# Optimization experiments

Measured on AMD Instinct MI355X. Metric: run time of the kernel, lower is better.

The kernel has to match this reference:

```python
import jax, jax.numpy as jnp
import numpy as np

K, D = 512, 64
B, H, W = 32, 64, 64


def setup_inputs() -> dict:
    key = jax.random.key(0)
    k1, k2 = jax.random.split(key)
    z_e_x = jax.random.normal(k1, (B, D, H, W), dtype=jnp.float32)
    # nn.Embedding weight initialized uniform(-1/K, 1/K)
    codebook = jax.random.uniform(k2, (K, D), dtype=jnp.float32,
                                  minval=-1.0 / K, maxval=1.0 / K)
    return {"z_e_x": z_e_x, "codebook": codebook}


def _quantize_indices(flat, codebook):
    # distances[n,k] = ||c_k||^2 + ||x_n||^2 - 2 x_n . c_k  (addmm form)
    cb_sqr = jnp.sum(codebook * codebook, axis=1)            # [K]
    x_sqr = jnp.sum(flat * flat, axis=1, keepdims=True)      # [N,1]
    distances = cb_sqr + x_sqr - 2.0 * (flat @ codebook.T)   # [N,K]
    return jnp.argmin(distances, axis=1)                     # [N]


def reference(z_e_x, codebook):
    # VQEmbedding.straight_through forward: returns (z_q_x, z_q_x_bar), both NCHW.
    b, d, h, w = z_e_x.shape
    x = jnp.transpose(z_e_x, (0, 2, 3, 1))       # NHWC
    flat = x.reshape(-1, d)                      # [N,D]
    idx = _quantize_indices(flat, codebook)      # [N]
    codes = jnp.take(codebook, idx, axis=0).reshape(b, h, w, d)
    z_q = jnp.transpose(codes, (0, 3, 1, 2))     # NCHW
    # z_q_x (detached codebook path) and z_q_x_bar (live codebook path) are
    # numerically identical in the forward pass.
    return (z_q, z_q)
```

## Files before the change

### kernel.cpp

```cpp
#include <hip/hip_runtime.h>


typedef short bf16x8 __attribute__((ext_vector_type(8)));
typedef float f32x4  __attribute__((ext_vector_type(4)));

#define KCODES 512
#define DDIM 64
#define HWSZ 4096
#define NPOS 131072
#define POSB 128
#define NBLK (NPOS / POSB)
#define OUT2_OFF 8388608
#define S_X 129

__device__ __forceinline__ unsigned short f2bf_rne(float f) {
    unsigned u = __builtin_bit_cast(unsigned, f);
    unsigned r = u + 0x7FFFu + ((u >> 16) & 1u);
    return (unsigned short)(r >> 16);
}
__device__ __forceinline__ float bf2f(unsigned short h) {
    unsigned u = ((unsigned)h) << 16;
    return __builtin_bit_cast(float, u);
}

__device__ __forceinline__ float np_sumsq64(const float* __restrict__ a) {
#pragma clang fp contract(off)
    float r0 = a[0]*a[0], r1 = a[1]*a[1], r2 = a[2]*a[2], r3 = a[3]*a[3];
    float r4 = a[4]*a[4], r5 = a[5]*a[5], r6 = a[6]*a[6], r7 = a[7]*a[7];
#pragma unroll
    for (int i = 8; i < 64; i += 8) {
        r0 += a[i+0]*a[i+0]; r1 += a[i+1]*a[i+1];
        r2 += a[i+2]*a[i+2]; r3 += a[i+3]*a[i+3];
        r4 += a[i+4]*a[i+4]; r5 += a[i+5]*a[i+5];
        r6 += a[i+6]*a[i+6]; r7 += a[i+7]*a[i+7];
    }
    return ((r0+r1)+(r2+r3)) + ((r4+r5)+(r6+r7));
}

__global__ __launch_bounds__(256) void vq_prep(
    const float* __restrict__ cb, unsigned short* __restrict__ wsb,
    float* __restrict__ wscb)
{
    if (blockIdx.x < 128) {
        int u = blockIdx.x * 256 + threadIdx.x;
        int k = u >> 6, d = u & 63;
        float c = cb[u];
        unsigned short ch = f2bf_rne(c);
        float clf = c - bf2f(ch);
        unsigned short cl = f2bf_rne(clf);
        int tile = k >> 4, n = k & 15;
        int chunk = d >> 5, quad = (d >> 3) & 3, j = d & 7;
        int lane = quad * 16 + n;
        size_t base = ((((size_t)tile*2 + chunk)*2 + 0)*64 + lane)*8 + j;
        wsb[base]       = (unsigned short)ch;
        wsb[base + 512] = (unsigned short)cl;
    } else {
        int k = (blockIdx.x - 128) * 256 + threadIdx.x;
        if (k < KCODES) wscb[k] = np_sumsq64(cb + k * DDIM);
    }
}

__global__ __launch_bounds__(256, 4) void vq_main(
    const float* __restrict__ z, const float* __restrict__ cb,
    const unsigned short* __restrict__ wsb, const float* __restrict__ wscb,
    float* __restrict__ out)
{
#pragma clang fp contract(off)
    __shared__ float s_regA[64 * S_X];
    __shared__ float s_cbsqr[KCODES];
    __shared__ float s_xsqr[POSB];
    __shared__ float s_part[2 * POSB];
    __shared__ int   s_idx[POSB];
    __shared__ int   s_flist[POSB];
    __shared__ int   s_cnt;

    const int tid = threadIdx.x;
    const int wv = tid >> 6, ln = tid & 63;
    const int m = ln & 15, q = ln >> 4;
    const int n0 = blockIdx.x * POSB;
    const long gbase = (long)(n0 >> 12) * (DDIM * HWSZ) + (n0 & 4095);

    if (tid == 0) s_cnt = 0;
    s_cbsqr[tid] = wscb[tid];
    s_cbsqr[tid + 256] = wscb[tid + 256];

#pragma unroll
    for (int i = 0; i < 32; ++i) {
        int d = wv * 16 + (i & 15), ph = i >> 4;
        s_regA[d * S_X + ph * 64 + ln] = z[gbase + (long)d * HWSZ + ph * 64 + ln];
    }
    __syncthreads();

    {
        int p = tid & 127, h = tid >> 7;
        float r0 = 0.f, r1 = 0.f, r2 = 0.f, r3 = 0.f;
#pragma unroll
        for (int i = 0; i < 8; ++i) {
            float a0 = s_regA[(8*i + 4*h + 0) * S_X + p];
            float a1 = s_regA[(8*i + 4*h + 1) * S_X + p];
            float a2 = s_regA[(8*i + 4*h + 2) * S_X + p];
            float a3 = s_regA[(8*i + 4*h + 3) * S_X + p];
            r0 += a0*a0; r1 += a1*a1; r2 += a2*a2; r3 += a3*a3;
        }
        s_part[h * POSB + p] = (r0 + r1) + (r2 + r3);
    }

    bf16x8 Ah[4], Al[4];
#pragma unroll
    for (int rt = 0; rt < 2; ++rt)
#pragma unroll
        for (int c = 0; c < 2; ++c) {
            int pos = wv * 32 + rt * 16 + m;
            bf16x8 ah, al;
#pragma unroll
            for (int j = 0; j < 8; ++j) {
                float xv = s_regA[(c*32 + q*8 + j) * S_X + pos];
                unsigned short hh = f2bf_rne(xv);
                float lo = xv - bf2f(hh);
                ah[j] = (short)hh;
                al[j] = (short)f2bf_rne(lo);
            }
            Ah[rt*2 + c] = ah; Al[rt*2 + c] = al;
        }
    __syncthreads();
    if (tid < POSB) s_xsqr[tid] = s_part[tid] + s_part[POSB + tid];

    float m1[8], m2[8]; int t1[8];
#pragma unroll
    for (int i = 0; i < 8; ++i) { m1[i] = 3.4e38f; m2[i] = 3.4e38f; t1[i] = 0; }

    for (int g = 0; g < 4; ++g) {
        __syncthreads();
        const float4* src = (const float4*)wsb + g * 2048;
        float4* dst = (float4*)s_regA;
#pragma unroll
        for (int i = 0; i < 8; ++i) dst[i * 256 + tid] = src[i * 256 + tid];
        __syncthreads();

        const unsigned short* sb = (const unsigned short*)s_regA;
        for (int ti = 0; ti < 8; ++ti) {
            int t = g * 8 + ti;
            bf16x8 Bh0 = *(const bf16x8*)(sb + ((ti*2+0)*2+0)*512 + ln*8);
            bf16x8 Bl0 = *(const bf16x8*)(sb + ((ti*2+0)*2+1)*512 + ln*8);
            bf16x8 Bh1 = *(const bf16x8*)(sb + ((ti*2+1)*2+0)*512 + ln*8);
            bf16x8 Bl1 = *(const bf16x8*)(sb + ((ti*2+1)*2+1)*512 + ln*8);
            float cbv = s_cbsqr[t * 16 + m];
#pragma unroll
            for (int rt = 0; rt < 2; ++rt) {
                f32x4 acc = {0.f, 0.f, 0.f, 0.f};
                acc = __builtin_amdgcn_mfma_f32_16x16x32_bf16(Al[rt*2+0], Bh0, acc, 0,0,0);
                acc = __builtin_amdgcn_mfma_f32_16x16x32_bf16(Ah[rt*2+0], Bl0, acc, 0,0,0);
                acc = __builtin_amdgcn_mfma_f32_16x16x32_bf16(Ah[rt*2+0], Bh0, acc, 0,0,0);
                acc = __builtin_amdgcn_mfma_f32_16x16x32_bf16(Al[rt*2+1], Bh1, acc, 0,0,0);
                acc = __builtin_amdgcn_mfma_f32_16x16x32_bf16(Ah[rt*2+1], Bl1, acc, 0,0,0);
                acc = __builtin_amdgcn_mfma_f32_16x16x32_bf16(Ah[rt*2+1], Bh1, acc, 0,0,0);
#pragma unroll
                for (int r = 0; r < 4; ++r) {
                    float sc = fmaf(-2.f, acc[r], cbv);
                    int cell = rt * 4 + r;
                    bool lt = sc < m1[cell];
                    m2[cell] = fminf(m2[cell], lt ? m1[cell] : sc);
                    if (lt) { m1[cell] = sc; t1[cell] = t; }
                }
            }
        }
    }

#pragma unroll
    for (int cell = 0; cell < 8; ++cell) {
        int rt = cell >> 2, r = cell & 3;
        float v1 = m1[cell], v2 = m2[cell];
        int i1 = t1[cell] * 16 + m;
#pragma unroll
        for (int s = 1; s < 16; s <<= 1) {
            float o1 = __shfl_xor(v1, s);
            float o2 = __shfl_xor(v2, s);
            int   oi = __shfl_xor(i1, s);
            bool take = (o1 < v1) || (o1 == v1 && oi < i1);
            float lose = take ? v1 : o1;
            if (take) { v1 = o1; i1 = oi; }
            v2 = fminf(fminf(v2, o2), lose);
        }
        if (m == 0) {
            int pos = wv * 32 + rt * 16 + q * 4 + r;
            float xs = s_xsqr[pos];
            float sx = 8.0f * sqrtf(xs) * 1.01f;
            float amax = 0.00196f * sx + 0.01f;
            float eps = 1.5f * (3.0f * 1.52587890625e-5f * 0.00196f * sx
                                + 500.f * 5.96e-8f * amax);
            float delta = 2.4e-7f * (xs + 1.0f) + 64.f * 1.2e-7f * amax;
            float W = 2.f * eps + 2.f * delta + 1e-9f;
            int flag = (v2 - v1 <= W) ? (1 << 30) : 0;
            s_idx[pos] = i1 | flag;
        }
    }
    __syncthreads();
    if (tid < POSB) {
        if (s_idx[tid] & (1 << 30)) {
            int slot = atomicAdd(&s_cnt, 1);
            s_flist[slot] = tid;
        }
    }
    __syncthreads();

    const int cnt = s_cnt;
    for (int i = wv; i < cnt; i += 4) {
        int p = __builtin_amdgcn_readfirstlane(s_flist[i]);
        float xv = z[gbase + (long)ln * HWSZ + p];
        float xs = s_xsqr[p];
        float dot[8];
#pragma unroll
        for (int j = 0; j < 8; ++j) dot[j] = 0.f;
        const float* crow = cb + (ln * 8) * DDIM;
        for (int dc = 0; dc < 16; ++dc) {
            float x0 = __shfl(xv, dc*4 + 0);
            float x1 = __shfl(xv, dc*4 + 1);
            float x2 = __shfl(xv, dc*4 + 2);
            float x3 = __shfl(xv, dc*4 + 3);
#pragma unroll
            for (int j = 0; j < 8; ++j) {
                float4 cv = *(const float4*)(crow + j * DDIM + dc * 4);
                dot[j] = fmaf(x0, cv.x, dot[j]);
                dot[j] = fmaf(x1, cv.y, dot[j]);
                dot[j] = fmaf(x2, cv.z, dot[j]);
                dot[j] = fmaf(x3, cv.w, dot[j]);
            }
        }
        float bv = 3.4e38f; int bi = 0;
#pragma unroll
        for (int j = 0; j < 8; ++j) {
            int k = ln * 8 + j;
            float tt = s_cbsqr[k] + xs;
            float e = fmaf(-2.f, dot[j], tt);
            if (e < bv) { bv = e; bi = k; }
        }
#pragma unroll
        for (int s = 1; s < 64; s <<= 1) {
            float ov = __shfl_xor(bv, s); int oi = __shfl_xor(bi, s);
            if (ov < bv || (ov == bv && oi < bi)) { bv = ov; bi = oi; }
        }
        if (ln == 0) s_idx[p] = bi;
    }
    __syncthreads();

    {
        int p = tid & 127, hf = tid >> 7;
        int idx = s_idx[p] & 0x3FFFFFFF;
        const float4* crow4 = (const float4*)(cb + idx * DDIM + hf * 32);
        float* o0 = out + gbase + p;
        float* o1 = o0 + OUT2_OFF;
#pragma unroll
        for (int qq = 0; qq < 8; ++qq) {
            float4 v = crow4[qq];
            long db = (long)(hf * 32 + qq * 4) * HWSZ;
            o0[db]          = v.x; o0[db + HWSZ]   = v.y;
            o0[db + 2*HWSZ] = v.z; o0[db + 3*HWSZ] = v.w;
            o1[db]          = v.x; o1[db + HWSZ]   = v.y;
            o1[db + 2*HWSZ] = v.z; o1[db + 3*HWSZ] = v.w;
        }
    }
}

extern "C" void kernel_launch(void* const* d_in, const int* in_sizes, int n_in,
                              void* d_out, int out_size, void* d_ws, size_t ws_size,
                              hipStream_t stream) {
    const float* z  = (const float*)d_in[0];
    const float* cb = (const float*)d_in[1];
    float* out = (float*)d_out;
    unsigned short* wsb = (unsigned short*)d_ws;
    float* wscb = (float*)((char*)d_ws + 131072);
    vq_prep<<<130, 256, 0, stream>>>(cb, wsb, wscb);
    vq_main<<<NBLK, 256, 0, stream>>>(z, cb, wsb, wscb, out);
}
```

Measured before the change: 175.1 us.

## Double-buffer codebook tiles via async global-to-LDS loads and split MFMA chains

Replaces the blocking load-then-sync copy of codebook tiles into shared memory with a double-buffered pipeline. Smaller half-size tiles are fetched directly into LDS with global_load_lds while the current tile is consumed. The three-term bf16 split product is also restructured into three independent MFMA accumulation chains that are summed afterwards, shortening the dependency chain. The change alters the summation order and so may shift results slightly. It relies on the async copy landing before the barrier, with no explicit wait on the load counter.

```diff
diff --git a/kernel.cpp b/kernel.cpp
--- a/kernel.cpp
+++ b/kernel.cpp
@@ -21,6 +21,12 @@
 __device__ __forceinline__ float bf2f(unsigned short h) {
     unsigned u = ((unsigned)h) << 16;
     return __builtin_bit_cast(float, u);
+}
+
+__device__ __forceinline__ void async_cp16(const void* g, void* l) {
+    __builtin_amdgcn_global_load_lds(
+        (const __attribute__((address_space(1))) unsigned int*)g,
+        (__attribute__((address_space(3))) unsigned int*)l, 16, 0, 0);
 }
 
 __device__ __forceinline__ float np_sumsq64(const float* __restrict__ a) {
@@ -129,17 +135,28 @@
 #pragma unroll
     for (int i = 0; i < 8; ++i) { m1[i] = 3.4e38f; m2[i] = 3.4e38f; t1[i] = 0; }
 
-    for (int g = 0; g < 4; ++g) {
-        __syncthreads();
-        const float4* src = (const float4*)wsb + g * 2048;
-        float4* dst = (float4*)s_regA;
-#pragma unroll
-        for (int i = 0; i < 8; ++i) dst[i * 256 + tid] = src[i * 256 + tid];
-        __syncthreads();
-
-        const unsigned short* sb = (const unsigned short*)s_regA;
-        for (int ti = 0; ti < 8; ++ti) {
-            int t = g * 8 + ti;
+    {
+        const float4* src = (const float4*)wsb + 0 * 1024;
+        char* dstb = (char*)s_regA + (wv * 64) * 16;
+#pragma unroll
+        for (int i = 0; i < 4; ++i)
+            async_cp16(src + i * 256 + tid, dstb + i * 4096);
+    }
+    __syncthreads();
+
+    for (int g = 0; g < 8; ++g) {
+        if (g < 7) {
+            const float4* src = (const float4*)wsb + (g + 1) * 1024;
+            char* dstb = (char*)s_regA + ((g + 1) & 1) * 16384 + (wv * 64) * 16;
+#pragma unroll
+            for (int i = 0; i < 4; ++i)
+                async_cp16(src + i * 256 + tid, dstb + i * 4096);
+        }
+        const unsigned short* sb =
+            (const unsigned short*)s_regA + (g & 1) * 8192;
+#pragma unroll 2
+        for (int ti = 0; ti < 4; ++ti) {
+            int t = g * 4 + ti;
             bf16x8 Bh0 = *(const bf16x8*)(sb + ((ti*2+0)*2+0)*512 + ln*8);
             bf16x8 Bl0 = *(const bf16x8*)(sb + ((ti*2+0)*2+1)*512 + ln*8);
             bf16x8 Bh1 = *(const bf16x8*)(sb + ((ti*2+1)*2+0)*512 + ln*8);
@@ -147,13 +164,14 @@
             float cbv = s_cbsqr[t * 16 + m];
 #pragma unroll
             for (int rt = 0; rt < 2; ++rt) {
-                f32x4 acc = {0.f, 0.f, 0.f, 0.f};
-                acc = __builtin_amdgcn_mfma_f32_16x16x32_bf16(Al[rt*2+0], Bh0, acc, 0,0,0);
-                acc = __builtin_amdgcn_mfma_f32_16x16x32_bf16(Ah[rt*2+0], Bl0, acc, 0,0,0);
-                acc = __builtin_amdgcn_mfma_f32_16x16x32_bf16(Ah[rt*2+0], Bh0, acc, 0,0,0);
-                acc = __builtin_amdgcn_mfma_f32_16x16x32_bf16(Al[rt*2+1], Bh1, acc, 0,0,0);
-                acc = __builtin_amdgcn_mfma_f32_16x16x32_bf16(Ah[rt*2+1], Bl1, acc, 0,0,0);
-                acc = __builtin_amdgcn_mfma_f32_16x16x32_bf16(Ah[rt*2+1], Bh1, acc, 0,0,0);
+                const f32x4 zac = {0.f, 0.f, 0.f, 0.f};
+                f32x4 aP = __builtin_amdgcn_mfma_f32_16x16x32_bf16(Al[rt*2+0], Bh0, zac, 0,0,0);
+                f32x4 aQ = __builtin_amdgcn_mfma_f32_16x16x32_bf16(Ah[rt*2+0], Bl0, zac, 0,0,0);
+                f32x4 aR = __builtin_amdgcn_mfma_f32_16x16x32_bf16(Ah[rt*2+0], Bh0, zac, 0,0,0);
+                aP = __builtin_amdgcn_mfma_f32_16x16x32_bf16(Al[rt*2+1], Bh1, aP, 0,0,0);
+                aQ = __builtin_amdgcn_mfma_f32_16x16x32_bf16(Ah[rt*2+1], Bl1, aQ, 0,0,0);
+                aR = __builtin_amdgcn_mfma_f32_16x16x32_bf16(Ah[rt*2+1], Bh1, aR, 0,0,0);
+                f32x4 acc = (aP + aQ) + aR;
 #pragma unroll
                 for (int r = 0; r < 4; ++r) {
                     float sc = fmaf(-2.f, acc[r], cbv);
@@ -164,6 +182,7 @@
                 }
             }
         }
+        __syncthreads();
     }
 
 #pragma unroll
```

Result: no change. 178.3 us (+1.8%).

## Restructure VQ kernel to single-wave blocks streaming codebook fragments from global

Applied to the files above, without the earlier changes.

Switches from 256-thread blocks of 128 positions to 64-thread single-wave blocks of 64 positions, each wave covering 4 row tiles. Codebook bf16 fragments are no longer staged in LDS with block barriers; they are loaded straight from global/L2 with one-tile-ahead register prefetch. The input tile is stored position-major with an XOR swizzle to avoid LDS bank conflicts. The three MFMA accumulators run as independent chains to break the dependency. Fallback rescoring now uses a ballot mask instead of an LDS atomic list. In exchange it uses many more registers, launches 4x more blocks, and each wave rereads the whole codebook fragment set from cache.

```diff
diff --git a/kernel.cpp b/kernel.cpp
--- a/kernel.cpp
+++ b/kernel.cpp
@@ -8,10 +8,9 @@
 #define DDIM 64
 #define HWSZ 4096
 #define NPOS 131072
-#define POSB 128
-#define NBLK (NPOS / POSB)
+#define POSW 64
+#define NBLK (NPOS / POSW)
 #define OUT2_OFF 8388608
-#define S_X 129
 
 __device__ __forceinline__ unsigned short f2bf_rne(float f) {
     unsigned u = __builtin_bit_cast(unsigned, f);
@@ -60,114 +59,116 @@
     }
 }
 
-__global__ __launch_bounds__(256, 4) void vq_main(
+__device__ __forceinline__ int xchunk(int p, int c) {
+    return p * 16 + (c ^ (p & 15));
+}
+
+__global__ __launch_bounds__(64, 2) void vq_main(
     const float* __restrict__ z, const float* __restrict__ cb,
     const unsigned short* __restrict__ wsb, const float* __restrict__ wscb,
     float* __restrict__ out)
 {
 #pragma clang fp contract(off)
-    __shared__ float s_regA[64 * S_X];
+    __shared__ float s_x[POSW * DDIM];
     __shared__ float s_cbsqr[KCODES];
-    __shared__ float s_xsqr[POSB];
-    __shared__ float s_part[2 * POSB];
-    __shared__ int   s_idx[POSB];
-    __shared__ int   s_flist[POSB];
-    __shared__ int   s_cnt;
-
-    const int tid = threadIdx.x;
-    const int wv = tid >> 6, ln = tid & 63;
+    __shared__ int   s_idx[POSW];
+
+    const int ln = threadIdx.x;
     const int m = ln & 15, q = ln >> 4;
-    const int n0 = blockIdx.x * POSB;
+    const int n0 = blockIdx.x * POSW;
     const long gbase = (long)(n0 >> 12) * (DDIM * HWSZ) + (n0 & 4095);
-
-    if (tid == 0) s_cnt = 0;
-    s_cbsqr[tid] = wscb[tid];
-    s_cbsqr[tid + 256] = wscb[tid + 256];
-
-#pragma unroll
-    for (int i = 0; i < 32; ++i) {
-        int d = wv * 16 + (i & 15), ph = i >> 4;
-        s_regA[d * S_X + ph * 64 + ln] = z[gbase + (long)d * HWSZ + ph * 64 + ln];
+    float4* s_x4 = (float4*)s_x;
+
+#pragma unroll
+    for (int i = 0; i < 8; ++i) s_cbsqr[i * 64 + ln] = wscb[i * 64 + ln];
+
+#pragma unroll
+    for (int c = 0; c < 16; ++c) {
+        float4 w;
+        w.x = z[gbase + (long)(4*c + 0) * HWSZ + ln];
+        w.y = z[gbase + (long)(4*c + 1) * HWSZ + ln];
+        w.z = z[gbase + (long)(4*c + 2) * HWSZ + ln];
+        w.w = z[gbase + (long)(4*c + 3) * HWSZ + ln];
+        s_x4[xchunk(ln, c)] = w;
     }
     __syncthreads();
 
+    float my_xsqr;
     {
-        int p = tid & 127, h = tid >> 7;
-        float r0 = 0.f, r1 = 0.f, r2 = 0.f, r3 = 0.f;
-#pragma unroll
-        for (int i = 0; i < 8; ++i) {
-            float a0 = s_regA[(8*i + 4*h + 0) * S_X + p];
-            float a1 = s_regA[(8*i + 4*h + 1) * S_X + p];
-            float a2 = s_regA[(8*i + 4*h + 2) * S_X + p];
-            float a3 = s_regA[(8*i + 4*h + 3) * S_X + p];
-            r0 += a0*a0; r1 += a1*a1; r2 += a2*a2; r3 += a3*a3;
-        }
-        s_part[h * POSB + p] = (r0 + r1) + (r2 + r3);
-    }
-
-    bf16x8 Ah[4], Al[4];
-#pragma unroll
-    for (int rt = 0; rt < 2; ++rt)
+        float r0=0.f,r1=0.f,r2=0.f,r3=0.f,r4=0.f,r5=0.f,r6=0.f,r7=0.f;
+#pragma unroll
+        for (int k = 0; k < 8; ++k) {
+            float4 A = s_x4[xchunk(ln, 2*k)];
+            float4 B = s_x4[xchunk(ln, 2*k + 1)];
+            r0 += A.x*A.x; r1 += A.y*A.y; r2 += A.z*A.z; r3 += A.w*A.w;
+            r4 += B.x*B.x; r5 += B.y*B.y; r6 += B.z*B.z; r7 += B.w*B.w;
+        }
+        my_xsqr = ((r0+r1)+(r2+r3)) + ((r4+r5)+(r6+r7));
+    }
+
+    bf16x8 Ah[8], Al[8];
+#pragma unroll
+    for (int rt = 0; rt < 4; ++rt)
 #pragma unroll
         for (int c = 0; c < 2; ++c) {
-            int pos = wv * 32 + rt * 16 + m;
+            int row = rt * 16 + m;
+            int h0 = c * 8 + q * 2;
+            float4 F0 = s_x4[xchunk(row, h0)];
+            float4 F1 = s_x4[xchunk(row, h0 + 1)];
+            float xv[8] = {F0.x,F0.y,F0.z,F0.w,F1.x,F1.y,F1.z,F1.w};
             bf16x8 ah, al;
 #pragma unroll
             for (int j = 0; j < 8; ++j) {
-                float xv = s_regA[(c*32 + q*8 + j) * S_X + pos];
-                unsigned short hh = f2bf_rne(xv);
-                float lo = xv - bf2f(hh);
+                unsigned short hh = f2bf_rne(xv[j]);
+                float lo = xv[j] - bf2f(hh);
                 ah[j] = (short)hh;
                 al[j] = (short)f2bf_rne(lo);
             }
             Ah[rt*2 + c] = ah; Al[rt*2 + c] = al;
         }
-    __syncthreads();
-    if (tid < POSB) s_xsqr[tid] = s_part[tid] + s_part[POSB + tid];
-
-    float m1[8], m2[8]; int t1[8];
-#pragma unroll
-    for (int i = 0; i < 8; ++i) { m1[i] = 3.4e38f; m2[i] = 3.4e38f; t1[i] = 0; }
-
-    for (int g = 0; g < 4; ++g) {
-        __syncthreads();
-        const float4* src = (const float4*)wsb + g * 2048;
-        float4* dst = (float4*)s_regA;
-#pragma unroll
-        for (int i = 0; i < 8; ++i) dst[i * 256 + tid] = src[i * 256 + tid];
-        __syncthreads();
-
-        const unsigned short* sb = (const unsigned short*)s_regA;
-        for (int ti = 0; ti < 8; ++ti) {
-            int t = g * 8 + ti;
-            bf16x8 Bh0 = *(const bf16x8*)(sb + ((ti*2+0)*2+0)*512 + ln*8);
-            bf16x8 Bl0 = *(const bf16x8*)(sb + ((ti*2+0)*2+1)*512 + ln*8);
-            bf16x8 Bh1 = *(const bf16x8*)(sb + ((ti*2+1)*2+0)*512 + ln*8);
-            bf16x8 Bl1 = *(const bf16x8*)(sb + ((ti*2+1)*2+1)*512 + ln*8);
-            float cbv = s_cbsqr[t * 16 + m];
-#pragma unroll
-            for (int rt = 0; rt < 2; ++rt) {
-                f32x4 acc = {0.f, 0.f, 0.f, 0.f};
-                acc = __builtin_amdgcn_mfma_f32_16x16x32_bf16(Al[rt*2+0], Bh0, acc, 0,0,0);
-                acc = __builtin_amdgcn_mfma_f32_16x16x32_bf16(Ah[rt*2+0], Bl0, acc, 0,0,0);
-                acc = __builtin_amdgcn_mfma_f32_16x16x32_bf16(Ah[rt*2+0], Bh0, acc, 0,0,0);
-                acc = __builtin_amdgcn_mfma_f32_16x16x32_bf16(Al[rt*2+1], Bh1, acc, 0,0,0);
-                acc = __builtin_amdgcn_mfma_f32_16x16x32_bf16(Ah[rt*2+1], Bl1, acc, 0,0,0);
-                acc = __builtin_amdgcn_mfma_f32_16x16x32_bf16(Ah[rt*2+1], Bh1, acc, 0,0,0);
-#pragma unroll
-                for (int r = 0; r < 4; ++r) {
-                    float sc = fmaf(-2.f, acc[r], cbv);
-                    int cell = rt * 4 + r;
-                    bool lt = sc < m1[cell];
-                    m2[cell] = fminf(m2[cell], lt ? m1[cell] : sc);
-                    if (lt) { m1[cell] = sc; t1[cell] = t; }
-                }
+
+    float m1[16], m2[16]; int t1[16];
+#pragma unroll
+    for (int i = 0; i < 16; ++i) { m1[i] = 3.4e38f; m2[i] = 3.4e38f; t1[i] = 0; }
+
+    const unsigned short* wb = wsb + ln * 8;
+#define LDFRAG(t, c, s) (*(const bf16x8*)(wb + ((((t)*2+(c))*2+(s)) << 9)))
+    bf16x8 Bh0 = LDFRAG(0,0,0), Bl0 = LDFRAG(0,0,1);
+    bf16x8 Bh1 = LDFRAG(0,1,0), Bl1 = LDFRAG(0,1,1);
+    float cbv = s_cbsqr[m];
+
+    for (int t = 0; t < 32; ++t) {
+        bf16x8 nh0, nl0, nh1, nl1; float ncbv = 0.f;
+        if (t < 31) {
+            nh0 = LDFRAG(t+1,0,0); nl0 = LDFRAG(t+1,0,1);
+            nh1 = LDFRAG(t+1,1,0); nl1 = LDFRAG(t+1,1,1);
+            ncbv = s_cbsqr[(t+1)*16 + m];
+        }
+#pragma unroll
+        for (int rt = 0; rt < 4; ++rt) {
+            const f32x4 zac = {0.f, 0.f, 0.f, 0.f};
+            f32x4 aP = __builtin_amdgcn_mfma_f32_16x16x32_bf16(Al[rt*2+0], Bh0, zac, 0,0,0);
+            f32x4 aQ = __builtin_amdgcn_mfma_f32_16x16x32_bf16(Ah[rt*2+0], Bl0, zac, 0,0,0);
+            f32x4 aR = __builtin_amdgcn_mfma_f32_16x16x32_bf16(Ah[rt*2+0], Bh0, zac, 0,0,0);
+            aP = __builtin_amdgcn_mfma_f32_16x16x32_bf16(Al[rt*2+1], Bh1, aP, 0,0,0);
+            aQ = __builtin_amdgcn_mfma_f32_16x16x32_bf16(Ah[rt*2+1], Bl1, aQ, 0,0,0);
+            aR = __builtin_amdgcn_mfma_f32_16x16x32_bf16(Ah[rt*2+1], Bh1, aR, 0,0,0);
+            f32x4 acc = (aP + aQ) + aR;
+#pragma unroll
+            for (int r = 0; r < 4; ++r) {
+                float sc = fmaf(-2.f, acc[r], cbv);
+                int cell = rt * 4 + r;
+                bool lt = sc < m1[cell];
+                m2[cell] = fminf(m2[cell], lt ? m1[cell] : sc);
+                if (lt) { m1[cell] = sc; t1[cell] = t; }
             }
         }
-    }
-
-#pragma unroll
-    for (int cell = 0; cell < 8; ++cell) {
+        Bh0 = nh0; Bl0 = nl0; Bh1 = nh1; Bl1 = nl1; cbv = ncbv;
+    }
+#undef LDFRAG
+
+#pragma unroll
+    for (int cell = 0; cell < 16; ++cell) {
         int rt = cell >> 2, r = cell & 3;
         float v1 = m1[cell], v2 = m2[cell];
         int i1 = t1[cell] * 16 + m;
@@ -181,33 +182,26 @@
             if (take) { v1 = o1; i1 = oi; }
             v2 = fminf(fminf(v2, o2), lose);
         }
-        if (m == 0) {
-            int pos = wv * 32 + rt * 16 + q * 4 + r;
-            float xs = s_xsqr[pos];
-            float sx = 8.0f * sqrtf(xs) * 1.01f;
-            float amax = 0.00196f * sx + 0.01f;
-            float eps = 1.5f * (3.0f * 1.52587890625e-5f * 0.00196f * sx
-                                + 500.f * 5.96e-8f * amax);
-            float delta = 2.4e-7f * (xs + 1.0f) + 64.f * 1.2e-7f * amax;
-            float W = 2.f * eps + 2.f * delta + 1e-9f;
-            int flag = (v2 - v1 <= W) ? (1 << 30) : 0;
-            s_idx[pos] = i1 | flag;
-        }
+        int pos = rt * 16 + q * 4 + r;
+        float xs = __shfl(my_xsqr, pos);
+        float sx = 8.0f * sqrtf(xs) * 1.01f;
+        float amax = 0.00196f * sx + 0.01f;
+        float eps = 1.5f * (3.0f * 1.52587890625e-5f * 0.00196f * sx
+                            + 500.f * 5.96e-8f * amax);
+        float delta = 2.4e-7f * (xs + 1.0f) + 64.f * 1.2e-7f * amax;
+        float W = 2.f * eps + 2.f * delta + 1e-9f;
+        int flag = (v2 - v1 <= W) ? (1 << 30) : 0;
+        if (m == 0) s_idx[pos] = i1 | flag;
     }
     __syncthreads();
-    if (tid < POSB) {
-        if (s_idx[tid] & (1 << 30)) {
-            int slot = atomicAdd(&s_cnt, 1);
-            s_flist[slot] = tid;
-        }
-    }
-    __syncthreads();
-
-    const int cnt = s_cnt;
-    for (int i = wv; i < cnt; i += 4) {
-        int p = __builtin_amdgcn_readfirstlane(s_flist[i]);
-        float xv = z[gbase + (long)ln * HWSZ + p];
-        float xs = s_xsqr[p];
+
+    int myidx = s_idx[ln];
+    unsigned long long mask = __ballot(myidx & (1 << 30));
+    while (mask) {
+        int p = __builtin_ctzll(mask);
+        mask &= mask - 1;
+        float xv = s_x[p * 64 + (((ln >> 2) ^ (p & 15)) << 2) + (ln & 3)];
+        float xs = __shfl(my_xsqr, p);
         float dot[8];
 #pragma unroll
         for (int j = 0; j < 8; ++j) dot[j] = 0.f;
@@ -244,15 +238,14 @@
     __syncthreads();
 
     {
-        int p = tid & 127, hf = tid >> 7;
-        int idx = s_idx[p] & 0x3FFFFFFF;
-        const float4* crow4 = (const float4*)(cb + idx * DDIM + hf * 32);
-        float* o0 = out + gbase + p;
+        int idx = s_idx[ln] & 0x3FFFFFFF;
+        const float4* crow4 = (const float4*)(cb + idx * DDIM);
+        float* o0 = out + gbase + ln;
         float* o1 = o0 + OUT2_OFF;
 #pragma unroll
-        for (int qq = 0; qq < 8; ++qq) {
-            float4 v = crow4[qq];
-            long db = (long)(hf * 32 + qq * 4) * HWSZ;
+        for (int c = 0; c < 16; ++c) {
+            float4 v = crow4[c];
+            long db = (long)(c * 4) * HWSZ;
             o0[db]          = v.x; o0[db + HWSZ]   = v.y;
             o0[db + 2*HWSZ] = v.z; o0[db + 3*HWSZ] = v.w;
             o1[db]          = v.x; o1[db + HWSZ]   = v.y;
@@ -270,5 +263,5 @@
     unsigned short* wsb = (unsigned short*)d_ws;
     float* wscb = (float*)((char*)d_ws + 131072);
     vq_prep<<<130, 256, 0, stream>>>(cb, wsb, wscb);
-    vq_main<<<NBLK, 256, 0, stream>>>(z, cb, wsb, wscb, out);
-}
+    vq_main<<<NBLK, 64, 0, stream>>>(z, cb, wsb, wscb, out);
+}
```

Result: slower. 187.4 us (+7.0%).
